# Kernel tuning notes

Hardware: AMD Instinct MI355X
Metric: run time of the kernel (lower is better)

The kernel has to match this reference:

```python
import jax, jax.numpy as jnp
import numpy as np

N_USERS, N_ITEMS = 100000, 100000
N_NODES = N_USERS + N_ITEMS
N_EDGES = 4000000
USER_DIM, ITEM_DIM = 256, 128
COMMON, HIDDEN, OUT = 64, 64, 32


def setup_inputs() -> dict:
    key = jax.random.key(0)
    ks = jax.random.split(key, 12)
    inp = {
        "user_tensor": jax.random.normal(ks[0], (N_USERS, USER_DIM), jnp.float32),
        "item_tensor": jax.random.normal(ks[1], (N_ITEMS, ITEM_DIM), jnp.float32),
        "edge_index": jax.random.randint(ks[2], (2, N_EDGES), 0, N_NODES, jnp.int64),
        "edge_weight": jax.random.uniform(ks[3], (N_EDGES,), jnp.float32),
        # user_proj / item_proj (nn.Linear: y = x @ W + b)
        "Wu": jax.random.normal(ks[4], (USER_DIM, COMMON), jnp.float32) / np.sqrt(USER_DIM),
        "bu": jnp.zeros((COMMON,), jnp.float32),
        "Wi": jax.random.normal(ks[5], (ITEM_DIM, COMMON), jnp.float32) / np.sqrt(ITEM_DIM),
        "bi": jnp.zeros((COMMON,), jnp.float32),
        # GCNConv layers (linear without bias + separate bias)
        "W1": jax.random.normal(ks[6], (COMMON, HIDDEN), jnp.float32) / np.sqrt(COMMON),
        "b1": jnp.zeros((HIDDEN,), jnp.float32),
        "W2": jax.random.normal(ks[7], (HIDDEN, OUT), jnp.float32) / np.sqrt(HIDDEN),
        "b2": jnp.zeros((OUT,), jnp.float32),
    }
    return inp


def gcn_conv(x, W, b, src, dst, ew, num_nodes):
    """PyG GCNConv: add self-loops (weight 1), symmetric deg norm, transform, scatter-add."""
    x = x @ W  # transform first: [N, out]
    loop = jnp.arange(num_nodes, dtype=src.dtype)
    src2 = jnp.concatenate([src, loop])
    dst2 = jnp.concatenate([dst, loop])
    ew2 = jnp.concatenate([ew, jnp.ones((num_nodes,), x.dtype)])
    deg = jax.ops.segment_sum(ew2, dst2, num_segments=num_nodes)
    dinv = jnp.where(deg > 0, jax.lax.rsqrt(deg), 0.0)
    norm = dinv[src2] * ew2 * dinv[dst2]  # [E+N]
    msgs = x[src2] * norm[:, None]  # gather + scale: [E+N, out]
    return jax.ops.segment_sum(msgs, dst2, num_segments=num_nodes) + b


def reference(user_tensor, item_tensor, edge_index, edge_weight,
              Wu, bu, Wi, bi, W1, b1, W2, b2):
    user_emb = user_tensor @ Wu + bu
    item_emb = item_tensor @ Wi + bi
    x = jnp.concatenate([user_emb, item_emb], axis=0)  # [N_NODES, COMMON]
    src, dst = edge_index[0], edge_index[1]
    x = gcn_conv(x, W1, b1, src, dst, edge_weight, N_NODES)
    x = jax.nn.relu(x)
    x = gcn_conv(x, W2, b2, src, dst, edge_weight, N_NODES)
    return x
```

## Files before the change

### kernel.cpp

```cpp
#include <hip/hip_runtime.h>
#include <hip/hip_bf16.h>

#define N_USERS_C 100000
#define N_ITEMS_C 100000
#define N_NODES_C 200000
#define USER_DIM_C 256
#define ITEM_DIM_C 128
#define COMMON_C 64
#define HIDDEN_C 64
#define OUT_DIM_C 32

#define CB_BITS 8
#define CB_NODES 256
#define NCB ((N_NODES_C + CB_NODES - 1) / CB_NODES)
#define CB_CAP 5632
#define B_THREADS 256
#define B_UNROLL (CB_CAP / B_THREADS)

#define BIN_GRID 512
#define BIN_CHUNK_MAX 8192
#define MAX_EPT 8

typedef unsigned int uint32;
typedef __bf16 bf16x8 __attribute__((ext_vector_type(8)));
typedef float f32x4 __attribute__((ext_vector_type(4)));



__device__ __forceinline__ float bf2f(ushort u) { return __uint_as_float(((unsigned)u) << 16); }
__device__ __forceinline__ ushort f2bf(float f) {
    unsigned u = __float_as_uint(f);
    return (ushort)((u + 0x7FFFu + ((u >> 16) & 1u)) >> 16);
}

union ABFrag {
    uint4 q;
    ushort u[8];
    bf16x8 v;
};


__global__ __launch_bounds__(1024) void bin_kernel(const int* __restrict__ src,
                                                   const int* __restrict__ dst,
                                                   const float* __restrict__ ew,
                                                   int* __restrict__ bucket_cnt,
                                                   uint2* __restrict__ rec2, int E, int chunk) {
    __shared__ int hist[NCB];
    __shared__ int cur[NCB];
    for (int i = threadIdx.x; i < NCB; i += 1024) hist[i] = 0;
    __syncthreads();
    const int beg = blockIdx.x * chunk;
    const int end = min(E, beg + chunk);

    int dc[MAX_EPT];
#pragma unroll
    for (int s = 0; s < MAX_EPT / 4; ++s) {
        const int e0 = beg + (threadIdx.x << 2) + (s << 12);
        int4 d4 = make_int4(-1, -1, -1, -1);
        if (e0 + 3 < end) {
            d4 = *(const int4*)(dst + e0);
        } else if (e0 < end) {
            d4.x = dst[e0];
            if (e0 + 1 < end) d4.y = dst[e0 + 1];
            if (e0 + 2 < end) d4.z = dst[e0 + 2];
        }
        dc[s * 4 + 0] = d4.x; dc[s * 4 + 1] = d4.y;
        dc[s * 4 + 2] = d4.z; dc[s * 4 + 3] = d4.w;
        if (d4.x >= 0) atomicAdd(&hist[d4.x >> CB_BITS], 1);
        if (d4.y >= 0) atomicAdd(&hist[d4.y >> CB_BITS], 1);
        if (d4.z >= 0) atomicAdd(&hist[d4.z >> CB_BITS], 1);
        if (d4.w >= 0) atomicAdd(&hist[d4.w >> CB_BITS], 1);
    }
    __syncthreads();

    for (int i = threadIdx.x; i < NCB; i += 1024) {
        const int h = hist[i];
        cur[i] = h ? atomicAdd(&bucket_cnt[i], h) : 0;
    }
    __syncthreads();

#pragma unroll
    for (int s = 0; s < MAX_EPT / 4; ++s) {
        const int e0 = beg + (threadIdx.x << 2) + (s << 12);
        if (e0 >= end) continue;
        int4 s4;
        float4 w4;
        if (e0 + 3 < end) {
            s4 = *(const int4*)(src + e0);
            w4 = *(const float4*)(ew + e0);
        } else {
            s4 = make_int4(0, 0, 0, 0);
            w4 = make_float4(0, 0, 0, 0);
            s4.x = src[e0]; w4.x = ew[e0];
            if (e0 + 1 < end) { s4.y = src[e0 + 1]; w4.y = ew[e0 + 1]; }
            if (e0 + 2 < end) { s4.z = src[e0 + 2]; w4.z = ew[e0 + 2]; }
        }
        const int dv[4] = {dc[s * 4 + 0], dc[s * 4 + 1], dc[s * 4 + 2], dc[s * 4 + 3]};
        const int sv[4] = {s4.x, s4.y, s4.z, s4.w};
        const float wv[4] = {w4.x, w4.y, w4.z, w4.w};
#pragma unroll
        for (int k = 0; k < 4; ++k) {
            const int d = dv[k];
            if (d < 0) continue;
            uint32 q = (uint32)(wv[k] * 255.0f + 0.5f);
            if (q > 255u) q = 255u;
            const int b = d >> CB_BITS;
            const int slot = atomicAdd(&cur[b], 1);
            if (slot < CB_CAP)
                rec2[(size_t)b * CB_CAP + slot] =
                    make_uint2((((uint32)sv[k]) << 8) | q, (uint32)d);
        }
    }
}


__global__ __launch_bounds__(B_THREADS) void region_build_kernel(
        const uint2* __restrict__ rec2, const int* __restrict__ bucket_cnt,
        uint32* __restrict__ csr32, int* __restrict__ row_beg,
        int* __restrict__ row_cnt, float* __restrict__ dinv) {
    __shared__ int pk[CB_NODES];
    __shared__ int s[CB_NODES];
    __shared__ int cur[CB_NODES];
    const int cb = blockIdx.x;
    const int node0 = cb << CB_BITS;
    int total = bucket_cnt[cb];
    if (total > CB_CAP) total = CB_CAP;
    const uint2* r = rec2 + (size_t)cb * CB_CAP;

    pk[threadIdx.x] = 0;
    __syncthreads();

    uint2 rr[B_UNROLL];
#pragma unroll
    for (int u = 0; u < B_UNROLL; ++u) {
        const int j = threadIdx.x + u * B_THREADS;
        if (j < total) {
            rr[u] = r[j];
            atomicAdd(&pk[rr[u].y & (CB_NODES - 1)],
                      (int)((1u << 20) | (rr[u].x & 255u)));
        } else {
            rr[u] = make_uint2(0u, 0xFFFFFFFFu);
        }
    }
    __syncthreads();

    const int v = pk[threadIdx.x] >> 20;
    s[threadIdx.x] = v;
    __syncthreads();
#pragma unroll
    for (int off = 1; off < CB_NODES; off <<= 1) {
        const int t = (threadIdx.x >= off) ? s[threadIdx.x - off] : 0;
        __syncthreads();
        s[threadIdx.x] += t;
        __syncthreads();
    }
    {
        const int ex = s[threadIdx.x] - v;
        const int node = node0 + threadIdx.x;
        const int abs0 = cb * (2 * CB_CAP) + ex;
        if (node < N_NODES_C) {
            row_beg[node] = abs0;
            row_cnt[node] = v;
            dinv[node] = rsqrtf(1.0f + (float)(pk[threadIdx.x] & 0xFFFFF) * (1.0f / 255.0f));
        }
        cur[threadIdx.x] = abs0;
    }
    __syncthreads();

#pragma unroll
    for (int u = 0; u < B_UNROLL; ++u) {
        if (rr[u].y != 0xFFFFFFFFu) {
            const int slot = atomicAdd(&cur[rr[u].y & (CB_NODES - 1)], 1);
            csr32[slot] = rr[u].x;
        }
    }
}


__device__ __forceinline__ void wt_one(const float* W, ushort* WT, int K, int N, int i) {
    int k = i / N, n = i % N;
    WT[(size_t)n * K + k] = f2bf(W[i]);
}

__global__ void wt_prep_kernel(const float* __restrict__ Wu, const float* __restrict__ Wi,
                               const float* __restrict__ W1, const float* __restrict__ W2,
                               ushort* __restrict__ wtU, ushort* __restrict__ wtI,
                               ushort* __restrict__ wt1, ushort* __restrict__ wt2) {
    const int SU = USER_DIM_C * 64, SI = ITEM_DIM_C * 64, S1 = 64 * 64, S2 = 64 * 32;
    int i = blockIdx.x * blockDim.x + threadIdx.x;
    if (i < SU) { wt_one(Wu, wtU, USER_DIM_C, 64, i); return; }
    i -= SU;
    if (i < SI) { wt_one(Wi, wtI, ITEM_DIM_C, 64, i); return; }
    i -= SI;
    if (i < S1) { wt_one(W1, wt1, 64, 64, i); return; }
    i -= S1;
    if (i < S2) wt_one(W2, wt2, 64, 32, i);
}

template <int K, int NT, bool XF32, bool SCALE>
__global__ __launch_bounds__(256) void mfma_proj_kernel(const void* __restrict__ Xv,
                                                        const ushort* __restrict__ WT,
                                                        const float* __restrict__ bias,
                                                        const float* __restrict__ dinvp,
                                                        ushort* __restrict__ Y, int M) {
    const int lane = threadIdx.x & 63;
    const int wave = threadIdx.x >> 6;
    const int lr = lane & 15;
    const int quad = lane >> 4;
    const int m0 = blockIdx.x * 64 + wave * 16;
    const int N = NT * 16;

    f32x4 acc[NT];
#pragma unroll
    for (int nt = 0; nt < NT; ++nt) acc[nt] = (f32x4){0.0f, 0.0f, 0.0f, 0.0f};

    int arow = m0 + lr;
    if (arow >= M) arow = M - 1;
    const size_t abase = (size_t)arow * K;

    for (int kc = 0; kc < K; kc += 32) {
        const int k0 = kc + quad * 8;
        ABFrag a;
        if (XF32) {
            const float* Xf = (const float*)Xv;
            float4 x0 = *(const float4*)(Xf + abase + k0);
            float4 x1 = *(const float4*)(Xf + abase + k0 + 4);
            a.u[0] = f2bf(x0.x); a.u[1] = f2bf(x0.y); a.u[2] = f2bf(x0.z); a.u[3] = f2bf(x0.w);
            a.u[4] = f2bf(x1.x); a.u[5] = f2bf(x1.y); a.u[6] = f2bf(x1.z); a.u[7] = f2bf(x1.w);
        } else {
            const ushort* Xb = (const ushort*)Xv;
            a.q = *(const uint4*)(Xb + abase + k0);
        }
#pragma unroll
        for (int nt = 0; nt < NT; ++nt) {
            ABFrag bf;
            bf.q = *(const uint4*)(WT + (size_t)(nt * 16 + lr) * K + k0);
            acc[nt] = __builtin_amdgcn_mfma_f32_16x16x32_bf16(a.v, bf.v, acc[nt], 0, 0, 0);
        }
    }

#pragma unroll
    for (int r = 0; r < 4; ++r) {
        const int m = m0 + quad * 4 + r;
        if (m < M) {
            const float sc = SCALE ? dinvp[m] : 1.0f;
#pragma unroll
            for (int nt = 0; nt < NT; ++nt) {
                const int n = nt * 16 + lr;
                const float bc = bias ? bias[n] : 0.0f;
                Y[(size_t)m * N + n] = f2bf((acc[nt][r] + bc) * sc);
            }
        }
    }
}


__device__ __forceinline__ void fma8(float* acc, const uint4 u, const float cv) {
    const uint32 w0 = u.x, w1 = u.y, w2 = u.z, w3 = u.w;
    acc[0] += __uint_as_float(w0 << 16) * cv;
    acc[1] += __uint_as_float(w0 & 0xFFFF0000u) * cv;
    acc[2] += __uint_as_float(w1 << 16) * cv;
    acc[3] += __uint_as_float(w1 & 0xFFFF0000u) * cv;
    acc[4] += __uint_as_float(w2 << 16) * cv;
    acc[5] += __uint_as_float(w2 & 0xFFFF0000u) * cv;
    acc[6] += __uint_as_float(w3 << 16) * cv;
    acc[7] += __uint_as_float(w3 & 0xFFFF0000u) * cv;
}

template <int N, bool RELU, typename TY>
__global__ __launch_bounds__(256) void gather_kernel(
        const int* __restrict__ row_beg, const int* __restrict__ row_cnt,
        const uint32* __restrict__ csr, const ushort* __restrict__ y,
        const float* __restrict__ dinv, const float* __restrict__ b,
        TY* __restrict__ out) {
    constexpr int COLS = 8;
    constexpr int LPN = N / COLS;
    const int node = blockIdx.x * (256 / LPN) + threadIdx.x / LPN;
    const int c0 = (threadIdx.x % LPN) * COLS;

    const int beg = row_beg[node];
    const int end = beg + row_cnt[node];

    float a0[COLS] = {}, a1[COLS] = {}, a2[COLS] = {}, a3[COLS] = {};
    int j = beg;
    for (; j + 4 <= end; j += 4) {
        const uint32 e0 = csr[j], e1 = csr[j + 1], e2 = csr[j + 2], e3 = csr[j + 3];
        const uint4 u0 = *(const uint4*)(y + ((size_t)(e0 >> 8)) * N + c0);
        const uint4 u1 = *(const uint4*)(y + ((size_t)(e1 >> 8)) * N + c0);
        const uint4 u2 = *(const uint4*)(y + ((size_t)(e2 >> 8)) * N + c0);
        const uint4 u3 = *(const uint4*)(y + ((size_t)(e3 >> 8)) * N + c0);
        const float c0v = (float)(e0 & 255u) * (1.0f / 255.0f);
        const float c1v = (float)(e1 & 255u) * (1.0f / 255.0f);
        const float c2v = (float)(e2 & 255u) * (1.0f / 255.0f);
        const float c3v = (float)(e3 & 255u) * (1.0f / 255.0f);
        fma8(a0, u0, c0v);
        fma8(a1, u1, c1v);
        fma8(a2, u2, c2v);
        fma8(a3, u3, c3v);
    }
    for (; j < end; ++j) {
        const uint32 e = csr[j];
        const uint4 u = *(const uint4*)(y + ((size_t)(e >> 8)) * N + c0);
        const float cv = (float)(e & 255u) * (1.0f / 255.0f);
        fma8(a0, u, cv);
    }

    const uint4 us = *(const uint4*)(y + (size_t)node * N + c0);
    fma8(a0, us, 1.0f);

    const float di = dinv[node];
    const float4 blo = *(const float4*)(b + c0);
    const float4 bhi = *(const float4*)(b + c0 + 4);
    float r[COLS];
#pragma unroll
    for (int c = 0; c < COLS; ++c) {
        r[c] = ((a0[c] + a1[c]) + (a2[c] + a3[c])) * di;
    }
    r[0] += blo.x; r[1] += blo.y; r[2] += blo.z; r[3] += blo.w;
    r[4] += bhi.x; r[5] += bhi.y; r[6] += bhi.z; r[7] += bhi.w;
    if (RELU) {
#pragma unroll
        for (int c = 0; c < COLS; ++c) r[c] = fmaxf(r[c], 0.0f);
    }
    TY* po = out + (size_t)node * N + c0;
    if constexpr (sizeof(TY) == 2) {
        ushort us8[8];
#pragma unroll
        for (int c = 0; c < COLS; ++c) us8[c] = f2bf(r[c]);
        *(uint4*)po = *(const uint4*)us8;
    } else {
        *(float4*)po = make_float4(r[0], r[1], r[2], r[3]);
        *(float4*)(po + 4) = make_float4(r[4], r[5], r[6], r[7]);
    }
}


extern "C" void kernel_launch(void* const* d_in, const int* in_sizes, int n_in,
                              void* d_out, int out_size, void* d_ws, size_t ws_size,
                              hipStream_t stream) {
    const float* user = (const float*)d_in[0];
    const float* item = (const float*)d_in[1];
    const int* ei = (const int*)d_in[2];
    const float* ew = (const float*)d_in[3];
    const float* Wu = (const float*)d_in[4];
    const float* bu = (const float*)d_in[5];
    const float* Wi = (const float*)d_in[6];
    const float* bi = (const float*)d_in[7];
    const float* W1 = (const float*)d_in[8];
    const float* b1 = (const float*)d_in[9];
    const float* W2 = (const float*)d_in[10];
    const float* b2 = (const float*)d_in[11];
    float* out = (float*)d_out;

    const int E = in_sizes[3];
    const int* src = ei;
    const int* dst = ei + E;
    const int NB = N_NODES_C;
    const int nblk = (E > BIN_GRID * BIN_CHUNK_MAX) ? ((E + BIN_CHUNK_MAX - 1) / BIN_CHUNK_MAX)
                                                    : BIN_GRID;
    const int chunk = (((E + nblk - 1) / nblk) + 3) & ~3;

    char* p = (char*)d_ws;
    uint2* rec2 = (uint2*)p;   p += (size_t)NCB * CB_CAP * 8;
    ushort* emb = (ushort*)p;  p += (size_t)NB * 64 * 2;
    ushort* y1 = (ushort*)p;   p += (size_t)NB * 64 * 2;
    ushort* h1 = (ushort*)p;   p += (size_t)NB * 64 * 2;
    ushort* y2 = (ushort*)p;   p += (size_t)NB * 32 * 2;
    int* bucket_cnt = (int*)p; p += (size_t)NCB * 4;
    int* row_beg = (int*)p;    p += (size_t)NB * 4;
    int* row_cnt = (int*)p;    p += (size_t)NB * 4;
    float* dinv = (float*)p;   p += (size_t)NB * 4;
    ushort* wtU = (ushort*)p;  p += (size_t)USER_DIM_C * 64 * 2;
    ushort* wtI = (ushort*)p;  p += (size_t)ITEM_DIM_C * 64 * 2;
    ushort* wt1 = (ushort*)p;  p += (size_t)64 * 64 * 2;
    ushort* wt2 = (ushort*)p;  p += (size_t)64 * 32 * 2;

    uint32* csr = (uint32*)rec2;

    hipMemsetAsync(bucket_cnt, 0, (size_t)NCB * 4, stream);
    bin_kernel<<<nblk, 1024, 0, stream>>>(src, dst, ew, bucket_cnt, rec2, E, chunk);
    region_build_kernel<<<NCB, B_THREADS, 0, stream>>>(rec2, bucket_cnt, csr, row_beg, row_cnt,
                                                       dinv);

    wt_prep_kernel<<<120, 256, 0, stream>>>(Wu, Wi, W1, W2, wtU, wtI, wt1, wt2);

    mfma_proj_kernel<USER_DIM_C, 4, true, false><<<(N_USERS_C + 63) / 64, 256, 0, stream>>>(
        user, wtU, bu, nullptr, emb, N_USERS_C);
    mfma_proj_kernel<ITEM_DIM_C, 4, true, false><<<(N_ITEMS_C + 63) / 64, 256, 0, stream>>>(
        item, wtI, bi, nullptr, emb + (size_t)N_USERS_C * 64, N_ITEMS_C);

    mfma_proj_kernel<64, 4, false, true><<<NB / 64, 256, 0, stream>>>(
        emb, wt1, (const float*)nullptr, dinv, y1, NB);
    gather_kernel<64, true><<<NB / 32, 256, 0, stream>>>(row_beg, row_cnt, csr, y1, dinv, b1, h1);

    mfma_proj_kernel<64, 2, false, true><<<NB / 64, 256, 0, stream>>>(
        h1, wt2, (const float*)nullptr, dinv, y2, NB);
    gather_kernel<32, false><<<NB / 64, 256, 0, stream>>>(row_beg, row_cnt, csr, y2, dinv, b2, out);
}
```

Measured before the change: 537.7 us.

## Sort CSR rows by source in shared memory and interleave four nodes per gather group

The region build now scatters edges into a shared-memory buffer and insertion-sorts each node's row by packed source key before writing it out coalesced. This gives the gathers a source-ordered access pattern, which should improve cache locality on y. The gather kernel now has each lane group process four nodes, interleaving their edge loops to raise memory-level parallelism and balance uneven degrees. In exchange it drops the four independent accumulators, and the serial per-thread insertion sort adds build time on high-degree rows.

```diff
diff --git a/kernel.cpp b/kernel.cpp
--- a/kernel.cpp
+++ b/kernel.cpp
@@ -119,8 +119,9 @@
         uint32* __restrict__ csr32, int* __restrict__ row_beg,
         int* __restrict__ row_cnt, float* __restrict__ dinv) {
     __shared__ int pk[CB_NODES];
-    __shared__ int s[CB_NODES];
+    __shared__ int sps[CB_NODES];
     __shared__ int cur[CB_NODES];
+    __shared__ uint32 ebuf[CB_CAP];
     const int cb = blockIdx.x;
     const int node0 = cb << CB_BITS;
     int total = bucket_cnt[cb];
@@ -145,25 +146,24 @@
     __syncthreads();
 
     const int v = pk[threadIdx.x] >> 20;
-    s[threadIdx.x] = v;
+    sps[threadIdx.x] = v;
     __syncthreads();
 #pragma unroll
     for (int off = 1; off < CB_NODES; off <<= 1) {
-        const int t = (threadIdx.x >= off) ? s[threadIdx.x - off] : 0;
+        const int t = (threadIdx.x >= off) ? sps[threadIdx.x - off] : 0;
         __syncthreads();
-        s[threadIdx.x] += t;
+        sps[threadIdx.x] += t;
         __syncthreads();
     }
+    const int ex = sps[threadIdx.x] - v;
     {
-        const int ex = s[threadIdx.x] - v;
         const int node = node0 + threadIdx.x;
-        const int abs0 = cb * (2 * CB_CAP) + ex;
         if (node < N_NODES_C) {
-            row_beg[node] = abs0;
+            row_beg[node] = cb * (2 * CB_CAP) + ex;
             row_cnt[node] = v;
             dinv[node] = rsqrtf(1.0f + (float)(pk[threadIdx.x] & 0xFFFFF) * (1.0f / 255.0f));
         }
-        cur[threadIdx.x] = abs0;
+        cur[threadIdx.x] = ex;
     }
     __syncthreads();
 
@@ -171,9 +171,24 @@
     for (int u = 0; u < B_UNROLL; ++u) {
         if (rr[u].y != 0xFFFFFFFFu) {
             const int slot = atomicAdd(&cur[rr[u].y & (CB_NODES - 1)], 1);
-            csr32[slot] = rr[u].x;
-        }
-    }
+            ebuf[slot] = rr[u].x;
+        }
+    }
+    __syncthreads();
+
+    for (int i = 1; i < v; ++i) {
+        const uint32 key = ebuf[ex + i];
+        int j = i - 1;
+        while (j >= 0 && ebuf[ex + j] > key) {
+            ebuf[ex + j + 1] = ebuf[ex + j];
+            --j;
+        }
+        ebuf[ex + j + 1] = key;
+    }
+    __syncthreads();
+
+    for (int j = threadIdx.x; j < total; j += B_THREADS)
+        csr32[(size_t)cb * (2 * CB_CAP) + j] = ebuf[j];
 }
 
 
@@ -275,62 +290,64 @@
         TY* __restrict__ out) {
     constexpr int COLS = 8;
     constexpr int LPN = N / COLS;
-    const int node = blockIdx.x * (256 / LPN) + threadIdx.x / LPN;
+    constexpr int NPG = 4;
+    constexpr int GPB = 256 / LPN;
+    const int g = threadIdx.x / LPN;
     const int c0 = (threadIdx.x % LPN) * COLS;
-
-    const int beg = row_beg[node];
-    const int end = beg + row_cnt[node];
-
-    float a0[COLS] = {}, a1[COLS] = {}, a2[COLS] = {}, a3[COLS] = {};
-    int j = beg;
-    for (; j + 4 <= end; j += 4) {
-        const uint32 e0 = csr[j], e1 = csr[j + 1], e2 = csr[j + 2], e3 = csr[j + 3];
-        const uint4 u0 = *(const uint4*)(y + ((size_t)(e0 >> 8)) * N + c0);
-        const uint4 u1 = *(const uint4*)(y + ((size_t)(e1 >> 8)) * N + c0);
-        const uint4 u2 = *(const uint4*)(y + ((size_t)(e2 >> 8)) * N + c0);
-        const uint4 u3 = *(const uint4*)(y + ((size_t)(e3 >> 8)) * N + c0);
-        const float c0v = (float)(e0 & 255u) * (1.0f / 255.0f);
-        const float c1v = (float)(e1 & 255u) * (1.0f / 255.0f);
-        const float c2v = (float)(e2 & 255u) * (1.0f / 255.0f);
-        const float c3v = (float)(e3 & 255u) * (1.0f / 255.0f);
-        fma8(a0, u0, c0v);
-        fma8(a1, u1, c1v);
-        fma8(a2, u2, c2v);
-        fma8(a3, u3, c3v);
-    }
-    for (; j < end; ++j) {
-        const uint32 e = csr[j];
-        const uint4 u = *(const uint4*)(y + ((size_t)(e >> 8)) * N + c0);
-        const float cv = (float)(e & 255u) * (1.0f / 255.0f);
-        fma8(a0, u, cv);
-    }
-
-    const uint4 us = *(const uint4*)(y + (size_t)node * N + c0);
-    fma8(a0, us, 1.0f);
-
-    const float di = dinv[node];
+    const int nbase = (blockIdx.x * GPB + g) * NPG;
+
+    int beg[NPG], cnt[NPG];
+    float acc[NPG][COLS] = {};
+    int kmax = 0;
+#pragma unroll
+    for (int i = 0; i < NPG; ++i) {
+        const int node = nbase + i;
+        const bool ok = node < N_NODES_C;
+        beg[i] = ok ? row_beg[node] : 0;
+        cnt[i] = ok ? row_cnt[node] : 0;
+        kmax = max(kmax, cnt[i]);
+    }
+
+    for (int k = 0; k < kmax; ++k) {
+#pragma unroll
+        for (int i = 0; i < NPG; ++i) {
+            if (k < cnt[i]) {
+                const uint32 e = csr[beg[i] + k];
+                const uint4 u = *(const uint4*)(y + ((size_t)(e >> 8)) * N + c0);
+                const float cv = (float)(e & 255u) * (1.0f / 255.0f);
+                fma8(acc[i], u, cv);
+            }
+        }
+    }
+
     const float4 blo = *(const float4*)(b + c0);
     const float4 bhi = *(const float4*)(b + c0 + 4);
-    float r[COLS];
-#pragma unroll
-    for (int c = 0; c < COLS; ++c) {
-        r[c] = ((a0[c] + a1[c]) + (a2[c] + a3[c])) * di;
-    }
-    r[0] += blo.x; r[1] += blo.y; r[2] += blo.z; r[3] += blo.w;
-    r[4] += bhi.x; r[5] += bhi.y; r[6] += bhi.z; r[7] += bhi.w;
-    if (RELU) {
-#pragma unroll
-        for (int c = 0; c < COLS; ++c) r[c] = fmaxf(r[c], 0.0f);
-    }
-    TY* po = out + (size_t)node * N + c0;
-    if constexpr (sizeof(TY) == 2) {
-        ushort us8[8];
-#pragma unroll
-        for (int c = 0; c < COLS; ++c) us8[c] = f2bf(r[c]);
-        *(uint4*)po = *(const uint4*)us8;
-    } else {
-        *(float4*)po = make_float4(r[0], r[1], r[2], r[3]);
-        *(float4*)(po + 4) = make_float4(r[4], r[5], r[6], r[7]);
+#pragma unroll
+    for (int i = 0; i < NPG; ++i) {
+        const int node = nbase + i;
+        if (node >= N_NODES_C) continue;
+        const uint4 us = *(const uint4*)(y + (size_t)node * N + c0);
+        fma8(acc[i], us, 1.0f);
+        const float di = dinv[node];
+        float r[COLS];
+#pragma unroll
+        for (int c = 0; c < COLS; ++c) r[c] = acc[i][c] * di;
+        r[0] += blo.x; r[1] += blo.y; r[2] += blo.z; r[3] += blo.w;
+        r[4] += bhi.x; r[5] += bhi.y; r[6] += bhi.z; r[7] += bhi.w;
+        if (RELU) {
+#pragma unroll
+            for (int c = 0; c < COLS; ++c) r[c] = fmaxf(r[c], 0.0f);
+        }
+        TY* po = out + (size_t)node * N + c0;
+        if constexpr (sizeof(TY) == 2) {
+            ushort us8[8];
+#pragma unroll
+            for (int c = 0; c < COLS; ++c) us8[c] = f2bf(r[c]);
+            *(uint4*)po = *(const uint4*)us8;
+        } else {
+            *(float4*)po = make_float4(r[0], r[1], r[2], r[3]);
+            *(float4*)(po + 4) = make_float4(r[4], r[5], r[6], r[7]);
+        }
     }
 }
 
@@ -391,9 +408,11 @@
 
     mfma_proj_kernel<64, 4, false, true><<<NB / 64, 256, 0, stream>>>(
         emb, wt1, (const float*)nullptr, dinv, y1, NB);
-    gather_kernel<64, true><<<NB / 32, 256, 0, stream>>>(row_beg, row_cnt, csr, y1, dinv, b1, h1);
+    gather_kernel<64, true><<<(NB + 127) / 128, 256, 0, stream>>>(row_beg, row_cnt, csr, y1,
+                                                                  dinv, b1, h1);
 
     mfma_proj_kernel<64, 2, false, true><<<NB / 64, 256, 0, stream>>>(
         h1, wt2, (const float*)nullptr, dinv, y2, NB);
-    gather_kernel<32, false><<<NB / 64, 256, 0, stream>>>(row_beg, row_cnt, csr, y2, dinv, b2, out);
-}
+    gather_kernel<32, false><<<(NB + 255) / 256, 256, 0, stream>>>(row_beg, row_cnt, csr, y2,
+                                                                   dinv, b2, out);
+}
```

Result: slower. 647.2 us (+20.3%).
